# Kernel optimization log

Hardware: AMD Instinct MI355X
Metric: run time of the kernel (lower is better)

Reference implementation:

```python
import jax, jax.numpy as jnp
import numpy as np

IN_DIM = 32
OUT_DIM = 32
VAR_DIM = 64
BATCH = 16384
KER_DIMS = [1024, 1024, 1024, 1024]
NUM_STEPS = 8  # fixed-step RK4 stand-in for adaptive odeint (tol=1e-4)


def setup_inputs() -> dict:
    key = jax.random.key(0)
    ks = jax.random.split(key, 12)
    x = jax.random.normal(ks[0], (BATCH, IN_DIM), dtype=jnp.float32)
    aug = jnp.ones((BATCH, VAR_DIM - IN_DIM), dtype=jnp.float32)
    dims = [VAR_DIM] + KER_DIMS + [VAR_DIM]
    inp = {"x": x, "aug": aug}
    for i, (d1, d2) in enumerate(zip(dims[:-1], dims[1:])):
        # Linear(d1+1, d2): weight (d2, d1+1), bias (d2,)
        inp[f"W{i}"] = jax.random.normal(ks[1 + 2 * i], (d2, d1 + 1), dtype=jnp.float32) * 0.02
        inp[f"b{i}"] = jax.random.normal(ks[2 + 2 * i], (d2,), dtype=jnp.float32) * 0.02
    return inp


def _odefunc(t, y, Ws, bs):
    # y: [B, VAR_DIM]; per-layer concat of scalar time column, Linear, ReLU (except last)
    out = y
    n = len(Ws)
    for i, (W, b) in enumerate(zip(Ws, bs)):
        z = jnp.concatenate([out, jnp.full((out.shape[0], 1), t, dtype=out.dtype)], axis=1)
        out = z @ W.T + b
        if i < n - 1:
            out = jax.nn.relu(out)
    return out


def _integrate(y0, Ws, bs):
    dt = jnp.float32(1.0 / NUM_STEPS)

    def rk4_step(y, t):
        k1 = _odefunc(t, y, Ws, bs)
        k2 = _odefunc(t + 0.5 * dt, y + 0.5 * dt * k1, Ws, bs)
        k3 = _odefunc(t + 0.5 * dt, y + 0.5 * dt * k2, Ws, bs)
        k4 = _odefunc(t + dt, y + dt * k3, Ws, bs)
        return y + (dt / 6.0) * (k1 + 2.0 * k2 + 2.0 * k3 + k4), None

    ts = jnp.arange(NUM_STEPS, dtype=jnp.float32) * dt
    y1, _ = jax.lax.scan(rk4_step, y0, ts)
    return y1


def reference(x, aug, W0, b0, W1, b1, W2, b2, W3, b3, W4, b4):
    Ws = (W0, W1, W2, W3, W4)
    bs = (b0, b1, b2, b3, b4)
    y0 = jnp.concatenate([x, aug], axis=1)  # [B, VAR_DIM]
    y1 = _integrate(y0, Ws, bs)
    return y1[:, :OUT_DIM]
```

## Files before the change

kernel.cpp:

```cpp
#include <hip/hip_runtime.h>
#include <cstdint>
#include <cstddef>

#define BATCH 16384

typedef float f32x4 __attribute__((ext_vector_type(4)));
typedef _Float16 f16x8 __attribute__((ext_vector_type(8)));

__device__ __forceinline__ unsigned short f2h_bits(float f) {
  _Float16 h = (_Float16)f;
  return __builtin_bit_cast(unsigned short, h);
}

__device__ __forceinline__ void async_cp16(const void* g, void* l) {
  __builtin_amdgcn_global_load_lds(
      (const __attribute__((address_space(1))) unsigned int*)g,
      (__attribute__((address_space(3))) unsigned int*)l, 16, 0, 0);
}

template <int BM, int BN, int WCOLS, int RT, int CT, int K, int N, bool RELU>
__launch_bounds__(256)
__global__ void gemm_h(const unsigned short* __restrict__ A,
                       const unsigned short* __restrict__ Bw,
                       const float* __restrict__ Wfull,
                       const float* __restrict__ bias,
                       float tval,
                       unsigned short* __restrict__ Ch) {
  constexpr int BK = 64;
  __shared__ __align__(16) unsigned short smA[BM * BK];
  __shared__ __align__(16) unsigned short smB[BN * BK];

  const int tid = threadIdx.x;
  const int wave = tid >> 6;
  const int lane = tid & 63;
  const int quad = lane >> 4;
  const int r16 = lane & 15;

  const int rowA0 = blockIdx.x * BM;
  const int rowB0 = blockIdx.y * BN;

  const int waveM = wave / WCOLS;
  const int waveN = wave % WCOLS;

  f32x4 acc[RT][CT];
  const f32x4 zero = {0.f, 0.f, 0.f, 0.f};
#pragma unroll
  for (int i = 0; i < RT; ++i)
#pragma unroll
    for (int j = 0; j < CT; ++j) acc[i][j] = zero;

  for (int k0 = 0; k0 < K; k0 += BK) {
#pragma unroll
    for (int i = 0; i < BM * 8 / 256; ++i) {
      const int s = i * 256 + tid;
      const int row = s >> 3;
      const int cp = s & 7;
      const int c = cp ^ (row & 7);
      const unsigned short* g = A + (size_t)(rowA0 + row) * K + (k0 + c * 8);
      char* l = ((char*)smA) + (size_t)(i * 256 + (wave << 6)) * 16;
      async_cp16(g, l);
    }
#pragma unroll
    for (int i = 0; i < BN * 8 / 256; ++i) {
      const int s = i * 256 + tid;
      const int row = s >> 3;
      const int cp = s & 7;
      const int c = cp ^ (row & 7);
      const unsigned short* g = Bw + (size_t)(rowB0 + row) * K + (k0 + c * 8);
      char* l = ((char*)smB) + (size_t)(i * 256 + (wave << 6)) * 16;
      async_cp16(g, l);
    }
    __syncthreads();

#pragma unroll
    for (int h = 0; h < 2; ++h) {
      f16x8 af[RT], bfr[CT];
#pragma unroll
      for (int mt = 0; mt < RT; ++mt) {
        const int row = (waveM * RT + mt) * 16 + r16;
        const int cp = (h * 4 + quad) ^ (row & 7);
        af[mt] = *(const f16x8*)(smA + row * BK + cp * 8);
      }
#pragma unroll
      for (int nt = 0; nt < CT; ++nt) {
        const int row = (waveN * CT + nt) * 16 + r16;
        const int cp = (h * 4 + quad) ^ (row & 7);
        bfr[nt] = *(const f16x8*)(smB + row * BK + cp * 8);
      }
#pragma unroll
      for (int mt = 0; mt < RT; ++mt)
#pragma unroll
        for (int nt = 0; nt < CT; ++nt)
          acc[mt][nt] =
              __builtin_amdgcn_mfma_f32_16x16x32_f16(af[mt], bfr[nt], acc[mt][nt], 0, 0, 0);
    }
    __syncthreads();
  }

  float* biasLds = (float*)smA;
  if (tid < BN) {
    const int col = rowB0 + tid;
    biasLds[tid] = bias[col] + tval * Wfull[(size_t)col * (K + 1) + K];
  }
  __syncthreads();

#pragma unroll
  for (int mt = 0; mt < RT; ++mt) {
    const int grow0 = rowA0 + (waveM * RT + mt) * 16 + quad * 4;
#pragma unroll
    for (int nt = 0; nt < CT; ++nt) {
      const int lcol = (waveN * CT + nt) * 16 + r16;
      const int gcol = rowB0 + lcol;
      const float bi = biasLds[lcol];
#pragma unroll
      for (int r = 0; r < 4; ++r) {
        float v = acc[mt][nt][r] + bi;
        if (RELU) v = fmaxf(v, 0.0f);
        Ch[(size_t)(grow0 + r) * N + gcol] = f2h_bits(v);
      }
    }
  }
}

__launch_bounds__(256)
__global__ void gemm_l4(const unsigned short* __restrict__ A,
                        const unsigned short* __restrict__ Bw,
                        const float* __restrict__ Wfull,
                        const float* __restrict__ bias,
                        float tval,
                        float* __restrict__ y, float* __restrict__ ksum,
                        unsigned short* __restrict__ yh,
                        float* __restrict__ outp, int mode, float dt) {
  constexpr int K = 1024, BK = 64, BM = 32, BN = 64;
  __shared__ __align__(16) unsigned short smA[BM * BK];
  __shared__ __align__(16) unsigned short smB[BN * BK];

  const int tid = threadIdx.x;
  const int wave = tid >> 6;
  const int lane = tid & 63;
  const int quad = lane >> 4;
  const int r16 = lane & 15;

  const int rowA0 = blockIdx.x * BM;
  const int waveM = wave >> 1;
  const int waveN = wave & 1;

  f32x4 acc[2];
  const f32x4 zero = {0.f, 0.f, 0.f, 0.f};
  acc[0] = zero; acc[1] = zero;

  for (int k0 = 0; k0 < K; k0 += BK) {
    {
      const int s = tid;
      const int row = s >> 3;
      const int cp = s & 7;
      const int c = cp ^ (row & 7);
      const unsigned short* g = A + (size_t)(rowA0 + row) * K + (k0 + c * 8);
      char* l = ((char*)smA) + (size_t)(wave << 6) * 16;
      async_cp16(g, l);
    }
#pragma unroll
    for (int i = 0; i < 2; ++i) {
      const int s = i * 256 + tid;
      const int row = s >> 3;
      const int cp = s & 7;
      const int c = cp ^ (row & 7);
      const unsigned short* g = Bw + (size_t)row * K + (k0 + c * 8);
      char* l = ((char*)smB) + (size_t)(i * 256 + (wave << 6)) * 16;
      async_cp16(g, l);
    }
    __syncthreads();

#pragma unroll
    for (int h = 0; h < 2; ++h) {
      f16x8 af, bfr[2];
      {
        const int row = waveM * 16 + r16;
        const int cp = (h * 4 + quad) ^ (row & 7);
        af = *(const f16x8*)(smA + row * BK + cp * 8);
      }
#pragma unroll
      for (int nt = 0; nt < 2; ++nt) {
        const int row = (waveN * 2 + nt) * 16 + r16;
        const int cp = (h * 4 + quad) ^ (row & 7);
        bfr[nt] = *(const f16x8*)(smB + row * BK + cp * 8);
      }
#pragma unroll
      for (int nt = 0; nt < 2; ++nt)
        acc[nt] = __builtin_amdgcn_mfma_f32_16x16x32_f16(af, bfr[nt], acc[nt], 0, 0, 0);
    }
    __syncthreads();
  }

  float* biasLds = (float*)smA;
  if (tid < BN) {
    biasLds[tid] = bias[tid] + tval * Wfull[(size_t)tid * (K + 1) + K];
  }
  __syncthreads();

  const int grow0 = rowA0 + waveM * 16 + quad * 4;
#pragma unroll
  for (int nt = 0; nt < 2; ++nt) {
    const int col = waveN * 32 + nt * 16 + r16;
    const float bi = biasLds[col];
#pragma unroll
    for (int r = 0; r < 4; ++r) {
      const float k = acc[nt][r] + bi;
      const int row = grow0 + r;
      const int idx = row * 64 + col;
      if (mode == 0) {
        ksum[idx] = k;
        yh[idx] = f2h_bits(y[idx] + 0.5f * dt * k);
      } else if (mode == 1) {
        ksum[idx] += 2.f * k;
        yh[idx] = f2h_bits(y[idx] + 0.5f * dt * k);
      } else if (mode == 2) {
        ksum[idx] += 2.f * k;
        yh[idx] = f2h_bits(y[idx] + dt * k);
      } else {
        const float yn = y[idx] + (dt / 6.f) * (ksum[idx] + k);
        y[idx] = yn;
        yh[idx] = f2h_bits(yn);
        if (outp && col < 32) outp[row * 32 + col] = yn;
      }
    }
  }
}

__global__ void conv_w(const float* __restrict__ W, unsigned short* __restrict__ Wh,
                       int N, int K) {
  const int idx = blockIdx.x * 256 + threadIdx.x;
  if (idx < N * K) {
    const int n = idx / K;
    const int k = idx - n * K;
    Wh[idx] = f2h_bits(W[(size_t)n * (K + 1) + k]);
  }
}

__global__ void init_y(const float* __restrict__ x, const float* __restrict__ aug,
                       float* __restrict__ y, unsigned short* __restrict__ yh) {
  const int idx = blockIdx.x * 256 + threadIdx.x;
  const int i = idx >> 6;
  const int j = idx & 63;
  const float v = (j < 32) ? x[i * 32 + j] : aug[i * 32 + (j - 32)];
  y[idx] = v;
  yh[idx] = f2h_bits(v);
}

extern "C" void kernel_launch(void* const* d_in, const int* in_sizes, int n_in,
                              void* d_out, int out_size, void* d_ws, size_t ws_size,
                              hipStream_t stream) {
  const float* x = (const float*)d_in[0];
  const float* aug = (const float*)d_in[1];
  const float* W[5];
  const float* b[5];
  for (int i = 0; i < 5; ++i) {
    W[i] = (const float*)d_in[2 + 2 * i];
    b[i] = (const float*)d_in[3 + 2 * i];
  }

  char* ws = (char*)d_ws;
  auto alloc = [&](size_t bytes) -> char* {
    char* p = ws;
    ws += (bytes + 255) & ~(size_t)255;
    return p;
  };
  float* y = (float*)alloc((size_t)BATCH * 64 * 4);
  unsigned short* yh = (unsigned short*)alloc((size_t)BATCH * 64 * 2);
  unsigned short* h1 = (unsigned short*)alloc((size_t)BATCH * 1024 * 2);
  unsigned short* h2 = (unsigned short*)alloc((size_t)BATCH * 1024 * 2);
  float* ksum = (float*)alloc((size_t)BATCH * 64 * 4);
  const int Kdim[5] = {64, 1024, 1024, 1024, 1024};
  const int Ndim[5] = {1024, 1024, 1024, 1024, 64};
  unsigned short* Wh[5];
  for (int i = 0; i < 5; ++i)
    Wh[i] = (unsigned short*)alloc((size_t)Ndim[i] * Kdim[i] * 2);

  for (int i = 0; i < 5; ++i) {
    const int total = Ndim[i] * Kdim[i];
    conv_w<<<(total + 255) / 256, 256, 0, stream>>>(W[i], Wh[i], Ndim[i], Kdim[i]);
  }
  init_y<<<BATCH * 64 / 256, 256, 0, stream>>>(x, aug, y, yh);

  const float dt = 0.125f;
  float* outp = (float*)d_out;

  auto eval = [&](float t, int mode, float* op) {
    gemm_h<128, 128, 2, 4, 4, 64, 1024, true>
        <<<dim3(BATCH / 128, 1024 / 128), 256, 0, stream>>>(
            yh, Wh[0], W[0], b[0], t, h1);
    unsigned short* src = h1;
    unsigned short* dst = h2;
    for (int L = 1; L <= 3; ++L) {
      gemm_h<128, 128, 2, 4, 4, 1024, 1024, true>
          <<<dim3(BATCH / 128, 1024 / 128), 256, 0, stream>>>(
              src, Wh[L], W[L], b[L], t, dst);
      unsigned short* tmp = src; src = dst; dst = tmp;
    }
    gemm_l4<<<dim3(BATCH / 32, 1), 256, 0, stream>>>(
        src, Wh[4], W[4], b[4], t, y, ksum, yh, op, mode, dt);
  };

  for (int s = 0; s < 8; ++s) {
    const float t0 = s * dt;
    eval(t0, 0, nullptr);
    eval(t0 + 0.5f * dt, 1, nullptr);
    eval(t0 + 0.5f * dt, 2, nullptr);
    eval(t0 + dt, 3, (s == 7) ? outp : nullptr);
  }
}
```

Baseline: 5.244 ms.

## Double-buffer LDS tiles with BK=32 and async prefetch in GEMM kernels

Both GEMM kernels now keep two LDS buffers with BK halved to 32. The next K-slice is issued through async global-to-LDS copies while MFMAs run on the current slice, which removes one barrier per iteration. The LDS swizzle is reworked for the 4-chunk rows, bias loading moves to a dedicated shared array at the top, and launch bounds now request 4 blocks per CU. This is meant to hide global load latency behind compute. In exchange it doubles the number of barrier iterations, and it relies on the single remaining barrier to order the async copies.

```diff
diff --git a/kernel.cpp b/kernel.cpp
--- a/kernel.cpp
+++ b/kernel.cpp
@@ -19,16 +19,18 @@
 }
 
 template <int BM, int BN, int WCOLS, int RT, int CT, int K, int N, bool RELU>
-__launch_bounds__(256)
+__launch_bounds__(256, 4)
 __global__ void gemm_h(const unsigned short* __restrict__ A,
                        const unsigned short* __restrict__ Bw,
                        const float* __restrict__ Wfull,
                        const float* __restrict__ bias,
                        float tval,
                        unsigned short* __restrict__ Ch) {
-  constexpr int BK = 64;
-  __shared__ __align__(16) unsigned short smA[BM * BK];
-  __shared__ __align__(16) unsigned short smB[BN * BK];
+  constexpr int BK = 32;
+  constexpr int NI = K / BK;
+  __shared__ __align__(16) unsigned short smA[2][BM * BK];
+  __shared__ __align__(16) unsigned short smB[2][BN * BK];
+  __shared__ float biasLds[BN];
 
   const int tid = threadIdx.x;
   const int wave = tid >> 6;
@@ -38,71 +40,71 @@
 
   const int rowA0 = blockIdx.x * BM;
   const int rowB0 = blockIdx.y * BN;
-
   const int waveM = wave / WCOLS;
   const int waveN = wave % WCOLS;
 
-  f32x4 acc[RT][CT];
-  const f32x4 zero = {0.f, 0.f, 0.f, 0.f};
-#pragma unroll
-  for (int i = 0; i < RT; ++i)
-#pragma unroll
-    for (int j = 0; j < CT; ++j) acc[i][j] = zero;
-
-  for (int k0 = 0; k0 < K; k0 += BK) {
-#pragma unroll
-    for (int i = 0; i < BM * 8 / 256; ++i) {
-      const int s = i * 256 + tid;
-      const int row = s >> 3;
-      const int cp = s & 7;
-      const int c = cp ^ (row & 7);
-      const unsigned short* g = A + (size_t)(rowA0 + row) * K + (k0 + c * 8);
-      char* l = ((char*)smA) + (size_t)(i * 256 + (wave << 6)) * 16;
-      async_cp16(g, l);
-    }
-#pragma unroll
-    for (int i = 0; i < BN * 8 / 256; ++i) {
-      const int s = i * 256 + tid;
-      const int row = s >> 3;
-      const int cp = s & 7;
-      const int c = cp ^ (row & 7);
-      const unsigned short* g = Bw + (size_t)(rowB0 + row) * K + (k0 + c * 8);
-      char* l = ((char*)smB) + (size_t)(i * 256 + (wave << 6)) * 16;
-      async_cp16(g, l);
-    }
-    __syncthreads();
-
-#pragma unroll
-    for (int h = 0; h < 2; ++h) {
-      f16x8 af[RT], bfr[CT];
-#pragma unroll
-      for (int mt = 0; mt < RT; ++mt) {
-        const int row = (waveM * RT + mt) * 16 + r16;
-        const int cp = (h * 4 + quad) ^ (row & 7);
-        af[mt] = *(const f16x8*)(smA + row * BK + cp * 8);
-      }
-#pragma unroll
-      for (int nt = 0; nt < CT; ++nt) {
-        const int row = (waveN * CT + nt) * 16 + r16;
-        const int cp = (h * 4 + quad) ^ (row & 7);
-        bfr[nt] = *(const f16x8*)(smB + row * BK + cp * 8);
-      }
-#pragma unroll
-      for (int mt = 0; mt < RT; ++mt)
-#pragma unroll
-        for (int nt = 0; nt < CT; ++nt)
-          acc[mt][nt] =
-              __builtin_amdgcn_mfma_f32_16x16x32_f16(af[mt], bfr[nt], acc[mt][nt], 0, 0, 0);
-    }
-    __syncthreads();
-  }
-
-  float* biasLds = (float*)smA;
   if (tid < BN) {
     const int col = rowB0 + tid;
     biasLds[tid] = bias[col] + tval * Wfull[(size_t)col * (K + 1) + K];
   }
-  __syncthreads();
+
+  auto stage = [&](int k0, int buf) {
+#pragma unroll
+    for (int i = 0; i < BM * 4 / 256; ++i) {
+      const int s = i * 256 + tid;
+      const int row = s >> 2;
+      const int c = (s & 3) ^ ((row >> 1) & 3);
+      const unsigned short* g = A + (size_t)(rowA0 + row) * K + (k0 + c * 8);
+      char* l = ((char*)smA[buf]) + (size_t)(i * 256 + (wave << 6)) * 16;
+      async_cp16(g, l);
+    }
+#pragma unroll
+    for (int i = 0; i < BN * 4 / 256; ++i) {
+      const int s = i * 256 + tid;
+      const int row = s >> 2;
+      const int c = (s & 3) ^ ((row >> 1) & 3);
+      const unsigned short* g = Bw + (size_t)(rowB0 + row) * K + (k0 + c * 8);
+      char* l = ((char*)smB[buf]) + (size_t)(i * 256 + (wave << 6)) * 16;
+      async_cp16(g, l);
+    }
+  };
+
+  f32x4 acc[RT][CT];
+  const f32x4 zero = {0.f, 0.f, 0.f, 0.f};
+#pragma unroll
+  for (int i = 0; i < RT; ++i)
+#pragma unroll
+    for (int j = 0; j < CT; ++j) acc[i][j] = zero;
+
+  stage(0, 0);
+
+#pragma unroll 2
+  for (int kk = 0; kk < NI; ++kk) {
+    __syncthreads();
+    if (kk + 1 < NI) stage((kk + 1) * BK, (kk + 1) & 1);
+
+    const unsigned short* sA = smA[kk & 1];
+    const unsigned short* sB = smB[kk & 1];
+    f16x8 af[RT], bfr[CT];
+#pragma unroll
+    for (int mt = 0; mt < RT; ++mt) {
+      const int row = (waveM * RT + mt) * 16 + r16;
+      const int cp = quad ^ ((row >> 1) & 3);
+      af[mt] = *(const f16x8*)(sA + row * BK + cp * 8);
+    }
+#pragma unroll
+    for (int nt = 0; nt < CT; ++nt) {
+      const int row = (waveN * CT + nt) * 16 + r16;
+      const int cp = quad ^ ((row >> 1) & 3);
+      bfr[nt] = *(const f16x8*)(sB + row * BK + cp * 8);
+    }
+#pragma unroll
+    for (int mt = 0; mt < RT; ++mt)
+#pragma unroll
+      for (int nt = 0; nt < CT; ++nt)
+        acc[mt][nt] =
+            __builtin_amdgcn_mfma_f32_16x16x32_f16(af[mt], bfr[nt], acc[mt][nt], 0, 0, 0);
+  }
 
 #pragma unroll
   for (int mt = 0; mt < RT; ++mt) {
@@ -122,7 +124,7 @@
   }
 }
 
-__launch_bounds__(256)
+__launch_bounds__(256, 4)
 __global__ void gemm_l4(const unsigned short* __restrict__ A,
                         const unsigned short* __restrict__ Bw,
                         const float* __restrict__ Wfull,
@@ -131,9 +133,10 @@
                         float* __restrict__ y, float* __restrict__ ksum,
                         unsigned short* __restrict__ yh,
                         float* __restrict__ outp, int mode, float dt) {
-  constexpr int K = 1024, BK = 64, BM = 32, BN = 64;
-  __shared__ __align__(16) unsigned short smA[BM * BK];
-  __shared__ __align__(16) unsigned short smB[BN * BK];
+  constexpr int K = 1024, BK = 32, BM = 32, BN = 64, NI = K / BK;
+  __shared__ __align__(16) unsigned short smA[2][BM * BK];
+  __shared__ __align__(16) unsigned short smB[2][BN * BK];
+  __shared__ float biasLds[BN];
 
   const int tid = threadIdx.x;
   const int wave = tid >> 6;
@@ -145,58 +148,58 @@
   const int waveM = wave >> 1;
   const int waveN = wave & 1;
 
+  if (tid < BN) {
+    biasLds[tid] = bias[tid] + tval * Wfull[(size_t)tid * (K + 1) + K];
+  }
+
+  auto stage = [&](int k0, int buf) {
+    if (tid < BM * 4) {
+      const int s = tid;
+      const int row = s >> 2;
+      const int c = (s & 3) ^ ((row >> 1) & 3);
+      const unsigned short* g = A + (size_t)(rowA0 + row) * K + (k0 + c * 8);
+      char* l = ((char*)smA[buf]) + (size_t)(wave << 6) * 16;
+      async_cp16(g, l);
+    }
+    {
+      const int s = tid;
+      const int row = s >> 2;
+      const int c = (s & 3) ^ ((row >> 1) & 3);
+      const unsigned short* g = Bw + (size_t)row * K + (k0 + c * 8);
+      char* l = ((char*)smB[buf]) + (size_t)(wave << 6) * 16;
+      async_cp16(g, l);
+    }
+  };
+
   f32x4 acc[2];
   const f32x4 zero = {0.f, 0.f, 0.f, 0.f};
   acc[0] = zero; acc[1] = zero;
 
-  for (int k0 = 0; k0 < K; k0 += BK) {
+  stage(0, 0);
+
+#pragma unroll 2
+  for (int kk = 0; kk < NI; ++kk) {
+    __syncthreads();
+    if (kk + 1 < NI) stage((kk + 1) * BK, (kk + 1) & 1);
+
+    const unsigned short* sA = smA[kk & 1];
+    const unsigned short* sB = smB[kk & 1];
+    f16x8 af, bfr[2];
     {
-      const int s = tid;
-      const int row = s >> 3;
-      const int cp = s & 7;
-      const int c = cp ^ (row & 7);
-      const unsigned short* g = A + (size_t)(rowA0 + row) * K + (k0 + c * 8);
-      char* l = ((char*)smA) + (size_t)(wave << 6) * 16;
-      async_cp16(g, l);
-    }
-#pragma unroll
-    for (int i = 0; i < 2; ++i) {
-      const int s = i * 256 + tid;
-      const int row = s >> 3;
-      const int cp = s & 7;
-      const int c = cp ^ (row & 7);
-      const unsigned short* g = Bw + (size_t)row * K + (k0 + c * 8);
-      char* l = ((char*)smB) + (size_t)(i * 256 + (wave << 6)) * 16;
-      async_cp16(g, l);
-    }
-    __syncthreads();
-
-#pragma unroll
-    for (int h = 0; h < 2; ++h) {
-      f16x8 af, bfr[2];
-      {
-        const int row = waveM * 16 + r16;
-        const int cp = (h * 4 + quad) ^ (row & 7);
-        af = *(const f16x8*)(smA + row * BK + cp * 8);
-      }
-#pragma unroll
-      for (int nt = 0; nt < 2; ++nt) {
-        const int row = (waveN * 2 + nt) * 16 + r16;
-        const int cp = (h * 4 + quad) ^ (row & 7);
-        bfr[nt] = *(const f16x8*)(smB + row * BK + cp * 8);
-      }
-#pragma unroll
-      for (int nt = 0; nt < 2; ++nt)
-        acc[nt] = __builtin_amdgcn_mfma_f32_16x16x32_f16(af, bfr[nt], acc[nt], 0, 0, 0);
-    }
-    __syncthreads();
-  }
-
-  float* biasLds = (float*)smA;
-  if (tid < BN) {
-    biasLds[tid] = bias[tid] + tval * Wfull[(size_t)tid * (K + 1) + K];
-  }
-  __syncthreads();
+      const int row = waveM * 16 + r16;
+      const int cp = quad ^ ((row >> 1) & 3);
+      af = *(const f16x8*)(sA + row * BK + cp * 8);
+    }
+#pragma unroll
+    for (int nt = 0; nt < 2; ++nt) {
+      const int row = (waveN * 2 + nt) * 16 + r16;
+      const int cp = quad ^ ((row >> 1) & 3);
+      bfr[nt] = *(const f16x8*)(sB + row * BK + cp * 8);
+    }
+#pragma unroll
+    for (int nt = 0; nt < 2; ++nt)
+      acc[nt] = __builtin_amdgcn_mfma_f32_16x16x32_f16(af, bfr[nt], acc[nt], 0, 0, 0);
+  }
 
   const int grow0 = rowA0 + waveM * 16 + quad * 4;
 #pragma unroll
```

After: 4.945 ms. 1.06x faster.
